# Kernel tuning notes

Hardware: AMD Instinct MI355X
Metric: run time of the kernel (lower is better)

The kernel has to match this reference:

```python
import jax, jax.numpy as jnp
import numpy as np

B, N, C = 64, 512, 1280


def setup_inputs() -> dict:
    key = jax.random.key(0)
    ks = jax.random.split(key, 10)
    scale = 0.02
    x = jax.random.normal(ks[0], (B, N, C), dtype=jnp.float32)
    Mask = jax.random.randint(ks[1], (B, N, N), 0, 2, dtype=jnp.int32)
    Wq = jax.random.normal(ks[2], (C, C), dtype=jnp.float32) * scale
    bq = jnp.zeros((C,), dtype=jnp.float32)
    Wk = jax.random.normal(ks[3], (C, C), dtype=jnp.float32) * scale
    bk = jnp.zeros((C,), dtype=jnp.float32)
    Wv = jax.random.normal(ks[4], (C, C), dtype=jnp.float32) * scale
    bv = jnp.zeros((C,), dtype=jnp.float32)
    Wr = jax.random.normal(ks[5], (C, C), dtype=jnp.float32) * scale
    br = jnp.zeros((C,), dtype=jnp.float32)
    return {"x": x, "Mask": Mask, "Wq": Wq, "bq": bq, "Wk": Wk, "bk": bk,
            "Wv": Wv, "bv": bv, "Wr": Wr, "br": br}


def reference(x, Mask, Wq, bq, Wk, bk, Wv, bv, Wr, br):
    # q, k, v: [B, N, C]
    q = x @ Wq + bq
    k = x @ Wk + bk
    v = x @ Wv + bv
    # scores[b, n, m] = q[b, n] . k[b, m]  -> [B, N, N]
    scores = jnp.einsum('bnc,bmc->bnm', q, k)
    # masked_fill BEFORE the scale divide, as in the original module
    scores = jnp.where(Mask == 0, jnp.float32(-1e20), scores)
    attn = jax.nn.softmax(scores / jnp.sqrt(jnp.float32(C)), axis=-1)
    # original: (V^T @ attn).permute -> out[b, n, c] = sum_m v[b, m, c] * attn[b, m, n]
    att_feat = jnp.einsum('bmc,bmn->bnc', v, attn)
    return att_feat @ Wr + br
```

## Files before the change

### kernel.cpp

```cpp
#include <hip/hip_runtime.h>
#include <hip/hip_bf16.h>

#define DI __device__ __forceinline__

typedef __attribute__((ext_vector_type(8))) short short8;
typedef __attribute__((ext_vector_type(4))) float f32x4;

DI unsigned short f2bf(float f) {
    union { float f; unsigned int u; } v; v.f = f;
    unsigned int r = v.u + 0x7FFFu + ((v.u >> 16) & 1u);
    return (unsigned short)(r >> 16);
}
DI float bf2f(unsigned short h) {
    union { unsigned int u; float f; } v; v.u = ((unsigned int)h) << 16;
    return v.f;
}

#define GLD16(g, l) __builtin_amdgcn_global_load_lds( \
    (const __attribute__((address_space(1))) void*)(g), \
    (__attribute__((address_space(3))) void*)(l), 16, 0, 0)

template<int EPI, int QKV>
__global__ __launch_bounds__(512, 2) void gemm256(
    const unsigned short* __restrict__ A, const unsigned short* __restrict__ Bt,
    void* __restrict__ Cout, const float* __restrict__ bias,
    const float* __restrict__ bias1, const float* __restrict__ bias2,
    int K, int lda, int ldb, int ldc,
    long sA, long sB, long sC)
{
    __shared__ unsigned short lds[65536];

    const unsigned gx = gridDim.x, gy = gridDim.y;
    unsigned lin = blockIdx.x + gx * (blockIdx.y + gy * blockIdx.z);
    const unsigned nwg = gx * gy * gridDim.z;
    lin = (lin & 7u) * (nwg >> 3) + (lin >> 3);
    int tn = lin % gx;
    const int tm = (lin / gx) % gy;
    const int z = lin / (gx * gy);

    int gsel = 0;
    if (QKV) {
        gsel = tn / 5; tn -= gsel * 5;
        Bt += (size_t)gsel * sB;
        Cout = (void*)((unsigned short*)Cout + (size_t)gsel * sC);
        if (gsel == 1) bias = bias1; else if (gsel == 2) bias = bias2;
    }

    const unsigned short* Ab = A + (long)z * sA + (size_t)(tm * 256) * lda;
    const unsigned short* Bb = Bt + (QKV ? 0 : (long)z * sB) + (size_t)(tn * 256) * ldb;

    const int tid = threadIdx.x, wave = tid >> 6, l = tid & 63;
    const int wr = wave >> 2, wc = wave & 3;

    const int srow = wave * 32 + (l >> 2);
    const int schunk = ((l & 3) ^ ((l >> 3) & 3)) * 8;
    const unsigned short* agS = Ab + (size_t)srow * lda + schunk;
    const unsigned short* bgS = Bb + (size_t)srow * ldb + schunk;
    unsigned short* ldsA0 = &lds[wave * 1024];
    unsigned short* ldsB0 = &lds[8192 + wave * 1024];

    const int rl = l & 15;
    const int cl8 = ((l >> 4) ^ ((l >> 1) & 3)) * 8;
    const int aoff = (wr * 128 + rl) * 32 + cl8;
    const int boff = 8192 + (wc * 64 + rl) * 32 + cl8;

#define REGOFF(buf, h) (((buf) * 2 + (h)) * 16384)
#define SA(t, h, buf) { const unsigned short* g_ = agS + (size_t)((t) * 64 + (h) * 32); \
    GLD16(g_, ldsA0 + REGOFF(buf, h)); \
    GLD16(g_ + (size_t)16 * lda, ldsA0 + REGOFF(buf, h) + 512); }
#define SB(t, h, buf) { const unsigned short* g_ = bgS + (size_t)((t) * 64 + (h) * 32); \
    GLD16(g_, ldsB0 + REGOFF(buf, h)); \
    GLD16(g_ + (size_t)16 * ldb, ldsB0 + REGOFF(buf, h) + 512); }

    f32x4 acc[8][4] = {};

#define PHASE(buf, h, STG, VMW) { \
    short8 af[8], bfv[4]; \
    _Pragma("unroll") for (int i = 0; i < 4; ++i) \
        af[i] = *(const short8*)&lds[REGOFF(buf, h) + aoff + i * 512]; \
    _Pragma("unroll") for (int n = 0; n < 4; ++n) \
        bfv[n] = *(const short8*)&lds[REGOFF(buf, h) + boff + n * 512]; \
    _Pragma("unroll") for (int i = 4; i < 8; ++i) \
        af[i] = *(const short8*)&lds[REGOFF(buf, h) + aoff + i * 512]; \
    STG; \
    __builtin_amdgcn_s_setprio(1); \
    _Pragma("unroll") for (int i = 0; i < 8; ++i) \
        _Pragma("unroll") for (int n = 0; n < 4; ++n) \
            acc[i][n] = __builtin_amdgcn_mfma_f32_16x16x32_bf16( \
                af[i], bfv[n], acc[i][n], 0, 0, 0); \
    __builtin_amdgcn_s_setprio(0); \
    asm volatile("s_waitcnt " VMW ::: "memory"); \
    __builtin_amdgcn_s_barrier(); \
  }

    SA(0, 0, 0); SB(0, 0, 0); SA(0, 1, 0); SB(0, 1, 0); SA(1, 0, 1); SB(1, 0, 1);
    asm volatile("s_waitcnt vmcnt(8)" ::: "memory");
    __builtin_amdgcn_s_barrier();

    const int NI = K >> 7;
    for (int j = 0; j < NI - 1; ++j) {
        const int t = 2 * j;
        PHASE(0, 0, SA(t + 1, 1, 1) SB(t + 1, 1, 1), "vmcnt(8)")
        PHASE(0, 1, SA(t + 2, 0, 0) SB(t + 2, 0, 0), "vmcnt(8)")
        PHASE(1, 0, SA(t + 2, 1, 0) SB(t + 2, 1, 0), "vmcnt(8)")
        PHASE(1, 1, SA(t + 3, 0, 1) SB(t + 3, 0, 1), "vmcnt(8)")
    }
    {
        const int t = 2 * (NI - 1);
        PHASE(0, 0, SA(t + 1, 1, 1) SB(t + 1, 1, 1), "vmcnt(8)")
        PHASE(0, 1, ((void)0),                       "vmcnt(4)")
        PHASE(1, 0, ((void)0),                       "vmcnt(0)")
        PHASE(1, 1, ((void)0),                       "vmcnt(0)")
    }
#undef PHASE
#undef SA
#undef SB
#undef REGOFF

    const long cb = QKV ? 0 : (long)z * sC;
    const int row0 = tm * 256 + wr * 128 + (l >> 4) * 4;
    const int col0 = tn * 256 + wc * 64 + rl;

    if (QKV && gsel == 2) {
        float b4[4];
        #pragma unroll
        for (int n = 0; n < 4; ++n) b4[n] = bias[col0 + n * 16];
        unsigned short* vout = (unsigned short*)Cout;
        const int bz = tm >> 1, mb = (tm & 1) * 256;
        #pragma unroll
        for (int hc = 0; hc < 2; ++hc) {
            if ((wc >> 1) == hc) {
                #pragma unroll
                for (int mi = 0; mi < 8; ++mi)
                    #pragma unroll
                    for (int n = 0; n < 4; ++n)
                        #pragma unroll
                        for (int r = 0; r < 4; ++r) {
                            const int lc = (wc & 1) * 64 + n * 16 + rl;
                            const int m  = wr * 128 + mi * 16 + ((l >> 4) << 2) + r;
                            lds[lc * 264 + m] = f2bf(acc[mi][n][r] + b4[n]);
                        }
            }
            __syncthreads();
            #pragma unroll
            for (int rr = 0; rr < 8; ++rr) {
                const int row = rr * 16 + (tid >> 5);
                const int ch = tid & 31;
                short8 vv = *(const short8*)&lds[row * 264 + ch * 8];
                __builtin_nontemporal_store(vv,
                    (short8*)&vout[(size_t)bz * 655360
                        + (size_t)(tn * 256 + hc * 128 + row) * 512 + mb + ch * 8]);
            }
            __syncthreads();
        }
    } else if (EPI == 0) {
        float b4[4];
        #pragma unroll
        for (int n = 0; n < 4; ++n) b4[n] = bias[col0 + n * 16];
        unsigned short* gout = (unsigned short*)Cout;
        #pragma unroll
        for (int half = 0; half < 2; ++half) {
            if (wr == half) {
                #pragma unroll
                for (int mi = 0; mi < 8; ++mi)
                    #pragma unroll
                    for (int n = 0; n < 4; ++n)
                        #pragma unroll
                        for (int r = 0; r < 4; ++r) {
                            const int lr = mi * 16 + ((l >> 4) << 2) + r;
                            const int lc = wc * 64 + n * 16 + rl;
                            lds[lr * 264 + lc] = f2bf(acc[mi][n][r] + b4[n]);
                        }
            }
            __syncthreads();
            const long rbase = (long)(tm * 256 + half * 128);
            #pragma unroll
            for (int rr = 0; rr < 8; ++rr) {
                const int row = rr * 16 + (tid >> 5);
                const int ch = tid & 31;
                short8 vv = *(const short8*)&lds[row * 264 + ch * 8];
                __builtin_nontemporal_store(vv,
                    (short8*)&gout[(rbase + row) * (size_t)ldc + tn * 256 + ch * 8]);
            }
            __syncthreads();
        }
    } else {
        #pragma unroll
        for (int mi = 0; mi < 8; ++mi) {
            #pragma unroll
            for (int n = 0; n < 4; ++n) {
                #pragma unroll
                for (int r = 0; r < 4; ++r) {
                    const int row = row0 + mi * 16 + r;
                    const int col = col0 + n * 16;
                    float v = acc[mi][n][r];
                    if (EPI == 3) v += bias[col];
                    if (EPI == 3)
                        __builtin_nontemporal_store(v, &((float*)Cout)[cb + (long)row * ldc + col]);
                    else
                        ((unsigned short*)Cout)[cb + (long)row * ldc + col] = f2bf(v);
                }
            }
        }
    }
}

__global__ __launch_bounds__(512, 2) void qk_softmax(
    const unsigned short* __restrict__ Q, const unsigned short* __restrict__ Km,
    unsigned short* __restrict__ Pt, const int* __restrict__ mask, float scale)
{
    __shared__ unsigned short lds[65536];

    const unsigned gx = gridDim.x;
    unsigned lin = blockIdx.x + gx * blockIdx.z;
    const unsigned nwg = gx * gridDim.z;
    lin = (lin & 7u) * (nwg >> 3) + (lin >> 3);
    const int tm = lin % gx;
    const int z  = lin / gx;

    const unsigned short* Ab = Q  + (size_t)z * 655360 + (size_t)(tm * 128) * 1280;
    const unsigned short* Bb = Km + (size_t)z * 655360;

    const int tid = threadIdx.x, wave = tid >> 6, l = tid & 63;
    const int wr = wave >> 2, wc = wave & 3;
    const int rl = l & 15, lh = l >> 4;

    const int schunk = ((l & 3) ^ ((l >> 3) & 3)) * 8;
    const unsigned short* agS = Ab + (size_t)(wave * 16 + (l >> 2)) * 1280 + schunk;
    const unsigned short* bgS = Bb + (size_t)(wave * 16 + (l >> 2)) * 1280 + schunk;
    unsigned short* ldsA = &lds[wave * 512];
    unsigned short* ldsB = &lds[4096 + wave * 512];

    const int cl8 = ((l >> 4) ^ ((l >> 1) & 3)) * 8;
    const int aoff = (wr * 64 + rl) * 32 + cl8;
    const int boff = 4096 + (wc * 128 + rl) * 32 + cl8;

#define SLOT(s) ((s) * 20480)
#define SAQ(t, s) { GLD16(agS + (size_t)(t) * 32, ldsA + SLOT(s)); }
#define SBQ(t, s) { const unsigned short* g_ = bgS + (size_t)(t) * 32; \
    GLD16(g_,                       ldsB + SLOT(s)); \
    GLD16(g_ + (size_t)128 * 1280,  ldsB + SLOT(s) + 4096); \
    GLD16(g_ + (size_t)256 * 1280,  ldsB + SLOT(s) + 8192); \
    GLD16(g_ + (size_t)384 * 1280,  ldsB + SLOT(s) + 12288); }

    f32x4 acc[4][8] = {};

    SAQ(0, 0) SBQ(0, 0) SAQ(1, 1) SBQ(1, 1)
    asm volatile("s_waitcnt vmcnt(5)" ::: "memory");
    __builtin_amdgcn_s_barrier();

    int g0 = 0;
    for (int t = 0; t < 40; ++t) {
        const int base = g0 * 20480;
        int g2 = g0 + 2; if (g2 >= 3) g2 -= 3;
        const bool stg = (t + 2 < 40);
        short8 af[4], bfv[8];
        #pragma unroll
        for (int i = 0; i < 4; ++i) af[i] = *(const short8*)&lds[base + aoff + i * 512];
        #pragma unroll
        for (int n = 0; n < 8; ++n) bfv[n] = *(const short8*)&lds[base + boff + n * 512];
        if (stg) { SAQ(t + 2, g2) SBQ(t + 2, g2) }
        __builtin_amdgcn_s_setprio(1);
        #pragma unroll
        for (int i = 0; i < 4; ++i)
            #pragma unroll
            for (int n = 0; n < 8; ++n)
                acc[i][n] = __builtin_amdgcn_mfma_f32_16x16x32_bf16(af[i], bfv[n], acc[i][n], 0, 0, 0);
        __builtin_amdgcn_s_setprio(0);
        if (stg) { asm volatile("s_waitcnt vmcnt(5)" ::: "memory"); }
        else     { asm volatile("s_waitcnt vmcnt(0)" ::: "memory"); }
        __builtin_amdgcn_s_barrier();
        g0 = (g0 == 2) ? 0 : g0 + 1;
    }
#undef SAQ
#undef SBQ
#undef SLOT

    const int col0 = wc * 128 + rl;
    {
        const int* mb = mask + (size_t)z * 262144;
        #pragma unroll
        for (int mi = 0; mi < 4; ++mi)
            #pragma unroll
            for (int r = 0; r < 4; ++r) {
                const int m = tm * 128 + wr * 64 + mi * 16 + lh * 4 + r;
                const int* mp = mb + (size_t)m * 512 + col0;
                #pragma unroll
                for (int nj = 0; nj < 8; ++nj) {
                    float x = acc[mi][nj][r] * scale;
                    if (mp[nj * 16] == 0) x = -2.795084971874737e18f;
                    acc[mi][nj][r] = x;
                }
            }
    }
    float* red = (float*)lds;
    float rmx[4][4], rinv[4][4];
    #pragma unroll
    for (int mi = 0; mi < 4; ++mi)
        #pragma unroll
        for (int r = 0; r < 4; ++r) {
            float mx = acc[mi][0][r];
            #pragma unroll
            for (int nj = 1; nj < 8; ++nj) mx = fmaxf(mx, acc[mi][nj][r]);
            mx = fmaxf(mx, __shfl_xor(mx, 1));
            mx = fmaxf(mx, __shfl_xor(mx, 2));
            mx = fmaxf(mx, __shfl_xor(mx, 4));
            mx = fmaxf(mx, __shfl_xor(mx, 8));
            if (rl == 0) red[wc * 128 + wr * 64 + mi * 16 + lh * 4 + r] = mx;
        }
    __syncthreads();
    #pragma unroll
    for (int mi = 0; mi < 4; ++mi)
        #pragma unroll
        for (int r = 0; r < 4; ++r) {
            const int rowl = wr * 64 + mi * 16 + lh * 4 + r;
            rmx[mi][r] = fmaxf(fmaxf(red[rowl], red[128 + rowl]),
                               fmaxf(red[256 + rowl], red[384 + rowl]));
        }
    __syncthreads();
    #pragma unroll
    for (int mi = 0; mi < 4; ++mi)
        #pragma unroll
        for (int r = 0; r < 4; ++r) {
            float s = 0.f;
            #pragma unroll
            for (int nj = 0; nj < 8; ++nj) {
                float e = __expf(acc[mi][nj][r] - rmx[mi][r]);
                acc[mi][nj][r] = e; s += e;
            }
            s += __shfl_xor(s, 1); s += __shfl_xor(s, 2);
            s += __shfl_xor(s, 4); s += __shfl_xor(s, 8);
            if (rl == 0) red[wc * 128 + wr * 64 + mi * 16 + lh * 4 + r] = s;
        }
    __syncthreads();
    #pragma unroll
    for (int mi = 0; mi < 4; ++mi)
        #pragma unroll
        for (int r = 0; r < 4; ++r) {
            const int rowl = wr * 64 + mi * 16 + lh * 4 + r;
            rinv[mi][r] = 1.0f / (red[rowl] + red[128 + rowl] + red[256 + rowl] + red[384 + rowl]);
        }
    unsigned short* Pb = Pt + (size_t)z * 262144 + (size_t)tm * 128;
    #pragma unroll
    for (int nh = 0; nh < 2; ++nh) {
        __syncthreads();
        if ((wc >> 1) == nh) {
            #pragma unroll
            for (int mi = 0; mi < 4; ++mi)
                #pragma unroll
                for (int nj = 0; nj < 8; ++nj)
                    #pragma unroll
                    for (int r = 0; r < 4; ++r) {
                        const int cl = (wc & 1) * 128 + nj * 16 + rl;
                        const int rowl = wr * 64 + mi * 16 + lh * 4 + r;
                        lds[cl * 132 + rowl] = f2bf(acc[mi][nj][r] * rinv[mi][r]);
                    }
        }
        __syncthreads();
        #pragma unroll
        for (int rr = 0; rr < 8; ++rr) {
            const int nl = rr * 32 + (tid >> 4);
            const int ch = tid & 15;
            short8 vv = *(const short8*)&lds[nl * 132 + ch * 8];
            *(short8*)&Pb[(size_t)(nh * 256 + nl) * 512 + ch * 8] = vv;
        }
    }
}

__global__ void transpose_w(const float* __restrict__ Wq, const float* __restrict__ Wk,
                            const float* __restrict__ Wv, const float* __restrict__ Wr,
                            unsigned short* __restrict__ Wt)
{
    const float* W = blockIdx.z == 0 ? Wq : blockIdx.z == 1 ? Wk : blockIdx.z == 2 ? Wv : Wr;
    unsigned short* dst = Wt + (size_t)blockIdx.z * 1280 * 1280;
    __shared__ float T[64][65];
    const int j0 = blockIdx.x * 64, k0 = blockIdx.y * 64;
    const int tid = threadIdx.x;
    for (int it = 0; it < 16; ++it) {
        int idx = it * 256 + tid;
        int r = idx >> 6, c = idx & 63;
        T[r][c] = W[(size_t)(k0 + r) * 1280 + j0 + c];
    }
    __syncthreads();
    for (int it = 0; it < 16; ++it) {
        int idx = it * 256 + tid;
        int r = idx >> 6, c = idx & 63;
        dst[(size_t)(j0 + r) * 1280 + k0 + c] = f2bf(T[c][r]);
    }
}

__global__ void cast_x(const float* __restrict__ x, unsigned short* __restrict__ xb, long n)
{
    long i = ((long)blockIdx.x * 256 + threadIdx.x) * 8;
    if (i + 8 > n) return;
    const float4* p = (const float4*)(x + i);
    float4 a = p[0], b = p[1];
    unsigned short o[8] = { f2bf(a.x), f2bf(a.y), f2bf(a.z), f2bf(a.w),
                            f2bf(b.x), f2bf(b.y), f2bf(b.z), f2bf(b.w) };
    *(short8*)(xb + i) = *(short8*)o;
}

extern "C" void kernel_launch(void* const* d_in, const int* in_sizes, int n_in,
                              void* d_out, int out_size, void* d_ws, size_t ws_size,
                              hipStream_t stream)
{
    const float* x   = (const float*)d_in[0];
    const int*  Mask = (const int*)d_in[1];
    const float* Wq  = (const float*)d_in[2];
    const float* bq  = (const float*)d_in[3];
    const float* Wk  = (const float*)d_in[4];
    const float* bk  = (const float*)d_in[5];
    const float* Wv  = (const float*)d_in[6];
    const float* bv  = (const float*)d_in[7];
    const float* Wr  = (const float*)d_in[8];
    const float* br  = (const float*)d_in[9];

    constexpr int N = 512, C = 1280;
    constexpr long MN = 32768;

    char* ws = (char*)d_ws;
    unsigned short* xb = (unsigned short*)ws;
    unsigned short* Wt = (unsigned short*)(ws + 83886080);
    unsigned short* Q  = (unsigned short*)(ws + 83886080 + 13107200);
    unsigned short* Km = Q + 41943040;
    unsigned short* VtD = Km + 41943040;
    unsigned short* Pt = VtD + 41943040;
    unsigned short* att = xb;

    const float scale = 0.02795084971874737f;

    transpose_w<<<dim3(20, 20, 4), 256, 0, stream>>>(Wq, Wk, Wv, Wr, Wt);
    cast_x<<<dim3(20480), 256, 0, stream>>>(x, xb, MN * C);

    gemm256<0, 1><<<dim3(15, 128, 1), 512, 0, stream>>>(xb, Wt, (void*)Q, bq, bk, bv,
        C, C, C, C, 0, 1638400L, 41943040L);

    qk_softmax<<<dim3(4, 1, 64), 512, 0, stream>>>(Q, Km, Pt, Mask, scale);

    gemm256<2, 0><<<dim3(5, 2, 64), 512, 0, stream>>>(Pt, VtD, (void*)att, nullptr, nullptr, nullptr,
        N, N, N, C, (long)N * N, (long)C * N, (long)N * C);

    gemm256<3, 0><<<dim3(5, 128, 1), 512, 0, stream>>>(att, Wt + 3 * 1638400, d_out, br, nullptr, nullptr,
        C, C, C, C, 0, 0, 0);
}
```

Before: 645.8 us.

## Fold output projection into value weights to eliminate final GEMM

Uses associativity to precompute Wv@Wr (and bv@Wr) once, so the value projection directly produces V·Wr. The attention-weighted sum then writes the final output with bias br, removing the separate 32768x1280x1280 output-projection GEMM and the att buffer round trip. It adds a small 1280^3 weight-fusion GEMM and a bias kernel per call, and gives up a bf16 rounding step on the intermediate attention features in exchange for one rounding of the fused weight.

```diff
diff --git a/kernel.cpp b/kernel.cpp
--- a/kernel.cpp
+++ b/kernel.cpp
@@ -26,14 +26,16 @@
     void* __restrict__ Cout, const float* __restrict__ bias,
     const float* __restrict__ bias1, const float* __restrict__ bias2,
     int K, int lda, int ldb, int ldc,
-    long sA, long sB, long sC)
+    long sA, long sB, long sC, int doswz)
 {
     __shared__ unsigned short lds[65536];
 
     const unsigned gx = gridDim.x, gy = gridDim.y;
     unsigned lin = blockIdx.x + gx * (blockIdx.y + gy * blockIdx.z);
-    const unsigned nwg = gx * gy * gridDim.z;
-    lin = (lin & 7u) * (nwg >> 3) + (lin >> 3);
+    if (doswz) {
+        const unsigned nwg = gx * gy * gridDim.z;
+        lin = (lin & 7u) * (nwg >> 3) + (lin >> 3);
+    }
     int tn = lin % gx;
     const int tm = (lin / gx) % gy;
     const int z = lin / (gx * gy);
@@ -369,13 +371,21 @@
 
 __global__ void transpose_w(const float* __restrict__ Wq, const float* __restrict__ Wk,
                             const float* __restrict__ Wv, const float* __restrict__ Wr,
-                            unsigned short* __restrict__ Wt)
+                            unsigned short* __restrict__ Wt, unsigned short* __restrict__ Wvb)
 {
     const float* W = blockIdx.z == 0 ? Wq : blockIdx.z == 1 ? Wk : blockIdx.z == 2 ? Wv : Wr;
+    const int j0 = blockIdx.x * 64, k0 = blockIdx.y * 64;
+    const int tid = threadIdx.x;
+    if (blockIdx.z == 2) {
+        for (int it = 0; it < 16; ++it) {
+            int idx = it * 256 + tid;
+            int r = idx >> 6, c = idx & 63;
+            Wvb[(size_t)(k0 + r) * 1280 + j0 + c] = f2bf(W[(size_t)(k0 + r) * 1280 + j0 + c]);
+        }
+        return;
+    }
     unsigned short* dst = Wt + (size_t)blockIdx.z * 1280 * 1280;
     __shared__ float T[64][65];
-    const int j0 = blockIdx.x * 64, k0 = blockIdx.y * 64;
-    const int tid = threadIdx.x;
     for (int it = 0; it < 16; ++it) {
         int idx = it * 256 + tid;
         int r = idx >> 6, c = idx & 63;
@@ -387,6 +397,15 @@
         int r = idx >> 6, c = idx & 63;
         dst[(size_t)(j0 + r) * 1280 + k0 + c] = f2bf(T[c][r]);
     }
+}
+
+__global__ void bias_vr(const float* __restrict__ bv, const float* __restrict__ Wr,
+                        float* __restrict__ bvr)
+{
+    const int cp = blockIdx.x * 256 + threadIdx.x;
+    float s = 0.f;
+    for (int c = 0; c < 1280; ++c) s += bv[c] * Wr[(size_t)c * 1280 + cp];
+    bvr[cp] = s;
 }
 
 __global__ void cast_x(const float* __restrict__ x, unsigned short* __restrict__ xb, long n)
@@ -419,27 +438,32 @@
     constexpr long MN = 32768;
 
     char* ws = (char*)d_ws;
-    unsigned short* xb = (unsigned short*)ws;
-    unsigned short* Wt = (unsigned short*)(ws + 83886080);
-    unsigned short* Q  = (unsigned short*)(ws + 83886080 + 13107200);
-    unsigned short* Km = Q + 41943040;
-    unsigned short* VtD = Km + 41943040;
-    unsigned short* Pt = VtD + 41943040;
-    unsigned short* att = xb;
+    unsigned short* xb  = (unsigned short*)ws;
+    unsigned short* Wt  = (unsigned short*)(ws + 83886080);
+    unsigned short* Wvb = (unsigned short*)(ws + 96993280);
+    float*          bvr = (float*)(ws + 100270080);
+    unsigned short* Q   = (unsigned short*)(ws + 100278272);
+    unsigned short* Km  = Q + 41943040;
+    unsigned short* Ut  = Km + 41943040;
+    unsigned short* Pt  = Ut + 41943040;
 
     const float scale = 0.02795084971874737f;
 
-    transpose_w<<<dim3(20, 20, 4), 256, 0, stream>>>(Wq, Wk, Wv, Wr, Wt);
+    transpose_w<<<dim3(20, 20, 4), 256, 0, stream>>>(Wq, Wk, Wv, Wr, Wt, Wvb);
+
+    gemm256<2, 0><<<dim3(5, 5, 1), 512, 0, stream>>>(Wt + 3 * 1638400, Wvb,
+        (void*)(Wt + 2 * 1638400), nullptr, nullptr, nullptr,
+        C, C, C, C, 0, 0, 0, 0);
+
+    bias_vr<<<dim3(5), 256, 0, stream>>>(bv, Wr, bvr);
+
     cast_x<<<dim3(20480), 256, 0, stream>>>(x, xb, MN * C);
 
-    gemm256<0, 1><<<dim3(15, 128, 1), 512, 0, stream>>>(xb, Wt, (void*)Q, bq, bk, bv,
-        C, C, C, C, 0, 1638400L, 41943040L);
+    gemm256<0, 1><<<dim3(15, 128, 1), 512, 0, stream>>>(xb, Wt, (void*)Q, bq, bk, bvr,
+        C, C, C, C, 0, 1638400L, 41943040L, 1);
 
     qk_softmax<<<dim3(4, 1, 64), 512, 0, stream>>>(Q, Km, Pt, Mask, scale);
 
-    gemm256<2, 0><<<dim3(5, 2, 64), 512, 0, stream>>>(Pt, VtD, (void*)att, nullptr, nullptr, nullptr,
-        N, N, N, C, (long)N * N, (long)C * N, (long)N * C);
-
-    gemm256<3, 0><<<dim3(5, 128, 1), 512, 0, stream>>>(att, Wt + 3 * 1638400, d_out, br, nullptr, nullptr,
-        C, C, C, C, 0, 0, 0);
-}
+    gemm256<3, 0><<<dim3(5, 2, 64), 512, 0, stream>>>(Pt, Ut, d_out, br, nullptr, nullptr,
+        N, N, N, C, (long)N * N, (long)C * N, (long)N * C, 1);
+}
```

Measured after the change: 662.8 us. 2.6% more time.
